# Kernel optimization log

Measured on AMD Instinct MI355X. Metric: run time of the kernel, lower is better.

Reference implementation:

```python
import jax, jax.numpy as jnp
import numpy as np

B, S, N_WIRES, EMBED_DIM, NUM_HEADS = 4, 2048, 8, 512, 8
D_K = EMBED_DIM // NUM_HEADS


def setup_inputs() -> dict:
    key = jax.random.key(0)
    k_x, k_th, k_q, k_k, k_v, k_c = jax.random.split(key, 6)
    x = jax.random.normal(k_x, (B, S, N_WIRES), dtype=jnp.float32)
    # trainable RX rotation angles, one per wire
    theta = jax.random.normal(k_th, (N_WIRES,), dtype=jnp.float32) * 0.1
    # nn.Linear(n_wires, embed_dim, bias=False) weights have shape (embed_dim, n_wires)
    sc_in = 1.0 / np.sqrt(N_WIRES)
    Wq = jax.random.normal(k_q, (EMBED_DIM, N_WIRES), dtype=jnp.float32) * sc_in
    Wk = jax.random.normal(k_k, (EMBED_DIM, N_WIRES), dtype=jnp.float32) * sc_in
    Wv = jax.random.normal(k_v, (EMBED_DIM, N_WIRES), dtype=jnp.float32) * sc_in
    Wc = jax.random.normal(k_c, (EMBED_DIM, EMBED_DIM), dtype=jnp.float32) * (1.0 / np.sqrt(EMBED_DIM))
    return {"x": x, "theta": theta, "Wq": Wq, "Wk": Wk, "Wv": Wv, "Wc": Wc}


def reference(x, theta, Wq, Wk, Wv, Wc):
    # Quantum encoding closed form: RX(x_i) then RX(theta_i) on |0> per wire gives <Z> = cos(x_i + theta_i).
    proj = jnp.cos(x + theta)  # (B, S, n_wires)
    b, s, _ = proj.shape
    q = jnp.einsum('bsn,en->bse', proj, Wq)
    k = jnp.einsum('bsn,en->bse', proj, Wk)
    v = jnp.einsum('bsn,en->bse', proj, Wv)
    # split heads: (B, H, S, d_k)
    q = q.reshape(b, s, NUM_HEADS, D_K).transpose(0, 2, 1, 3)
    k = k.reshape(b, s, NUM_HEADS, D_K).transpose(0, 2, 1, 3)
    v = v.reshape(b, s, NUM_HEADS, D_K).transpose(0, 2, 1, 3)
    scores = jnp.einsum('bhqd,bhkd->bhqk', q, k) / np.sqrt(D_K).astype(np.float32)
    attn = jax.nn.softmax(scores, axis=-1)  # dropout is identity at inference
    out = jnp.einsum('bhqk,bhkd->bhqd', attn, v)
    out = out.transpose(0, 2, 1, 3).reshape(b, s, EMBED_DIM)
    return jnp.einsum('bse,fe->bsf', out, Wc)
```

## Files before the change

### kernel.cpp

```cpp
#include <hip/hip_runtime.h>
#include <stdint.h>

#define N_B 4
#define S_LEN 2048
#define N_H 8
#define E_DIM 512

typedef __attribute__((ext_vector_type(8))) short bf16x8;
typedef __attribute__((ext_vector_type(4))) float f32x4;
typedef __attribute__((ext_vector_type(4))) unsigned int u32x4;
typedef __attribute__((ext_vector_type(2))) unsigned int u32x2;
typedef __attribute__((ext_vector_type(4))) unsigned short u16x4;
typedef __attribute__((ext_vector_type(8))) unsigned short u16x8;

#define MFMA16(a, b, c) __builtin_amdgcn_mfma_f32_16x16x32_bf16((a), (b), (c), 0, 0, 0)

__device__ __forceinline__ unsigned short f2bf(float f) {
    union { float f; unsigned int u; } v; v.f = f;
    unsigned int r = v.u + 0x7fffu + ((v.u >> 16) & 1u);
    return (unsigned short)(r >> 16);
}

__device__ __forceinline__ unsigned int pack2bf(float lo, float hi) {
    union { float f; unsigned int u; } a, b; a.f = lo; b.f = hi;
    return __builtin_amdgcn_perm(b.u + 0x8000u, a.u + 0x8000u, 0x07060302u);
}

__device__ __forceinline__ float fexp2(float x) {
#if __has_builtin(__builtin_amdgcn_exp2f)
    return __builtin_amdgcn_exp2f(x);
#else
    return exp2f(x);
#endif
}

#if __has_builtin(__builtin_amdgcn_permlane32_swap) && __has_builtin(__builtin_amdgcn_permlane16_swap)
#define HAVE_PERMLANE_SWAP 1
#endif

__device__ __forceinline__ void pl32(unsigned int& x, unsigned int& y) {
#ifdef HAVE_PERMLANE_SWAP
    auto r = __builtin_amdgcn_permlane32_swap(x, y, false, false);
    x = (unsigned int)r[0]; y = (unsigned int)r[1];
#else
    const int idx = (((int)threadIdx.x & 63) ^ 32) << 2;
    unsigned int xs = (unsigned int)__builtin_amdgcn_ds_bpermute(idx, (int)x);
    unsigned int ys = (unsigned int)__builtin_amdgcn_ds_bpermute(idx, (int)y);
    const bool lo = (threadIdx.x & 32) == 0;
    unsigned int nx = lo ? x : ys;
    unsigned int ny = lo ? xs : y;
    x = nx; y = ny;
#endif
}

__device__ __forceinline__ void pl16(unsigned int& x, unsigned int& y) {
#ifdef HAVE_PERMLANE_SWAP
    auto r = __builtin_amdgcn_permlane16_swap(x, y, false, false);
    x = (unsigned int)r[0]; y = (unsigned int)r[1];
#else
    unsigned int zs = (unsigned int)__builtin_amdgcn_ds_swizzle((int)y, 0x401F);
    unsigned int ws = (unsigned int)__builtin_amdgcn_ds_swizzle((int)x, 0x401F);
    const bool evenq = (threadIdx.x & 16) == 0;
    unsigned int nx = evenq ? x : zs;
    unsigned int ny = evenq ? ws : y;
    x = nx; y = ny;
#endif
}

#define Q_SCALE 0.18033688f

__global__ __launch_bounds__(256) void qkv_kernel(
    const float* __restrict__ x, const float* __restrict__ theta,
    const float* __restrict__ Wq, const float* __restrict__ Wk,
    const float* __restrict__ Wv,
    unsigned short* __restrict__ Q, unsigned short* __restrict__ K,
    unsigned short* __restrict__ Vt)
{
    __shared__ float proj[32][8];
    const int tid = threadIdx.x;
    const int mat = blockIdx.x % 3;
    const int chunk = blockIdx.x / 3;
    const int row0 = chunk * 32;
    const int b = row0 >> 11;
    const int s_in_b = row0 & (S_LEN - 1);

    proj[tid >> 3][tid & 7] = cosf(x[row0 * 8 + tid] + theta[tid & 7]);
    __syncthreads();

    if (mat < 2) {
        const float* W = (mat == 0) ? Wq : Wk;
        const float scale = (mat == 0) ? Q_SCALE : 1.0f;
        unsigned short* outp = (mat == 0) ? Q : K;
        const int eg = (tid & 127) * 4;
        const int sg = (tid >> 7) * 16;
        float w[4][8];
        #pragma unroll
        for (int e = 0; e < 4; ++e)
            #pragma unroll
            for (int n = 0; n < 8; ++n)
                w[e][n] = W[(eg + e) * 8 + n] * scale;
        const int h = eg >> 6, d0 = eg & 63;
        unsigned short* p0 = outp + ((size_t)(b * N_H + h) * S_LEN + s_in_b + sg) * 64 + d0;
        #pragma unroll 4
        for (int s = 0; s < 16; ++s) {
            f32x4 pa = *(const f32x4*)&proj[sg + s][0];
            f32x4 pc = *(const f32x4*)&proj[sg + s][4];
            u16x4 o;
            #pragma unroll
            for (int e = 0; e < 4; ++e) {
                float a = 0.f;
                #pragma unroll
                for (int n = 0; n < 4; ++n)
                    a += pa[n] * w[e][n] + pc[n] * w[e][n + 4];
                o[e] = f2bf(a);
            }
            *(u16x4*)&p0[s * 64] = o;
        }
    } else {
        f32x4 ps[8][2];
        const int sl0 = (tid & 3) * 8;
        #pragma unroll
        for (int k2 = 0; k2 < 8; ++k2) {
            ps[k2][0] = *(const f32x4*)&proj[sl0 + k2][0];
            ps[k2][1] = *(const f32x4*)&proj[sl0 + k2][4];
        }
        const int ecol = tid >> 2;
        for (int pass = 0; pass < 8; ++pass) {
            const int e = pass * 64 + ecol;
            const int h = e >> 6, dd = e & 63;
            float wr[8];
            #pragma unroll
            for (int n = 0; n < 8; ++n) wr[n] = Wv[e * 8 + n];
            u16x8 pk;
            #pragma unroll
            for (int k2 = 0; k2 < 8; ++k2) {
                float acc = 0.f;
                #pragma unroll
                for (int n = 0; n < 4; ++n)
                    acc += ps[k2][0][n] * wr[n] + ps[k2][1][n] * wr[n + 4];
                pk[k2] = f2bf(acc);
            }
            *(u16x8*)&Vt[((size_t)(b * N_H + h) * 64 + dd) * S_LEN + s_in_b + sl0] = pk;
        }
    }
}

__global__ __launch_bounds__(128) void flash_kernel(
    const unsigned short* __restrict__ Q, const unsigned short* __restrict__ K,
    const unsigned short* __restrict__ Vt, unsigned short* __restrict__ O)
{
    __shared__ short kt[2][64 * 72];
    __shared__ short vt[2][64 * 72];

    const int tid = threadIdx.x;
    const int lane = tid & 63, w = tid >> 6;
    const int quad = lane >> 4, lq = lane & 15;
    const int bid = (blockIdx.x & 7) * 64 + (blockIdx.x >> 3);
    const int qt = bid & 15, bh = bid >> 4;
    const int b = bh >> 3, h = bh & 7;

    const unsigned short* Qb = Q + (size_t)bh * S_LEN * 64;
    const unsigned short* Kb = K + (size_t)bh * S_LEN * 64;
    const unsigned short* Vb = Vt + (size_t)bh * 64 * S_LEN;

    bf16x8 qf[4][2];
    #pragma unroll
    for (int mt = 0; mt < 4; ++mt)
        #pragma unroll
        for (int ks = 0; ks < 2; ++ks)
            qf[mt][ks] = *(const bf16x8*)&Qb[(size_t)(qt * 128 + w * 64 + mt * 16 + lq) * 64 + ks * 32 + quad * 8];

    f32x4 oacc[4][4];
    #pragma unroll
    for (int mt = 0; mt < 4; ++mt)
        #pragma unroll
        for (int dt = 0; dt < 4; ++dt) oacc[mt][dt] = 0.f;
    float lsum[4] = {0.f, 0.f, 0.f, 0.f};

    u32x4 pkr[4], pvr[4];
    #pragma unroll
    for (int i = 0; i < 4; ++i) {
        const int u = tid + (i << 7);
        pkr[i] = *(const u32x4*)&Kb[(size_t)(u >> 3) * 64 + (u & 7) * 8];
        pvr[i] = *(const u32x4*)&Vb[(size_t)(u >> 3) * S_LEN + (u & 7) * 8];
    }
    #pragma unroll
    for (int i = 0; i < 4; ++i) {
        const int u = tid + (i << 7);
        *(u32x4*)&kt[0][(u >> 3) * 72 + (u & 7) * 8] = pkr[i];
        *(u32x4*)&vt[0][(u >> 3) * 72 + (u & 7) * 8] = pvr[i];
    }
    #pragma unroll
    for (int i = 0; i < 4; ++i) {
        const int u = tid + (i << 7);
        pkr[i] = *(const u32x4*)&Kb[(size_t)(64 + (u >> 3)) * 64 + (u & 7) * 8];
        pvr[i] = *(const u32x4*)&Vb[(size_t)(u >> 3) * S_LEN + 64 + (u & 7) * 8];
    }
    asm volatile("s_waitcnt lgkmcnt(0)" ::: "memory");
    __builtin_amdgcn_s_barrier();

    for (int kti = 0; kti < 32; ++kti) {
        const int cur = kti & 1, nxt = cur ^ 1;

        #pragma unroll
        for (int i = 0; i < 4; ++i) {
            const int u = tid + (i << 7);
            *(u32x4*)&kt[nxt][(u >> 3) * 72 + (u & 7) * 8] = pkr[i];
            *(u32x4*)&vt[nxt][(u >> 3) * 72 + (u & 7) * 8] = pvr[i];
        }
        const int kb2 = (kti < 30) ? (kti + 2) * 64 : 0;
        #pragma unroll
        for (int i = 0; i < 4; ++i) {
            const int u = tid + (i << 7);
            pkr[i] = *(const u32x4*)&Kb[(size_t)(kb2 + (u >> 3)) * 64 + (u & 7) * 8];
            pvr[i] = *(const u32x4*)&Vb[(size_t)(u >> 3) * S_LEN + kb2 + (u & 7) * 8];
        }

        const short* ktc = &kt[cur][0];
        const short* vtc = &vt[cur][0];

        #pragma unroll
        for (int ksub = 0; ksub < 2; ++ksub) {
            f32x4 sacc[4][2];
            #pragma unroll
            for (int mt = 0; mt < 4; ++mt)
                #pragma unroll
                for (int m2 = 0; m2 < 2; ++m2) sacc[mt][m2] = 0.f;
            #pragma unroll
            for (int m2 = 0; m2 < 2; ++m2) {
                #pragma unroll
                for (int ks = 0; ks < 2; ++ks) {
                    bf16x8 af = *(const bf16x8*)&ktc[((ksub * 2 + m2) * 16 + lq) * 72 + ks * 32 + quad * 8];
                    #pragma unroll
                    for (int mt = 0; mt < 4; ++mt)
                        sacc[mt][m2] = MFMA16(af, qf[mt][ks], sacc[mt][m2]);
                }
            }

            bf16x8 pa[4];
            #pragma unroll
            for (int mt = 0; mt < 4; ++mt) {
                unsigned int u_[2][2];
                #pragma unroll
                for (int m2 = 0; m2 < 2; ++m2) {
                    f32x4 p;
                    #pragma unroll
                    for (int e = 0; e < 4; ++e) p[e] = fexp2(sacc[mt][m2][e]);
                    lsum[mt] += (p[0] + p[1]) + (p[2] + p[3]);
                    u_[m2][0] = pack2bf(p[0], p[1]);
                    u_[m2][1] = pack2bf(p[2], p[3]);
                }
                union { unsigned int uu[4]; bf16x8 v; } A;
                #pragma unroll
                for (int wd = 0; wd < 2; ++wd) {
                    unsigned int a = u_[0][wd];
                    unsigned int c = u_[1][wd];
                    pl32(a, c);
                    pl16(a, c);
                    A.uu[wd] = a;
                    A.uu[2 + wd] = c;
                }
                pa[mt] = A.v;
            }

            #pragma unroll
            for (int dt = 0; dt < 4; ++dt) {
                bf16x8 bf = *(const bf16x8*)&vtc[(dt * 16 + lq) * 72 + ksub * 32 + quad * 8];
                #pragma unroll
                for (int mt = 0; mt < 4; ++mt)
                    oacc[mt][dt] = MFMA16(pa[mt], bf, oacc[mt][dt]);
            }
        }

        asm volatile("s_waitcnt lgkmcnt(0)" ::: "memory");
        __builtin_amdgcn_s_barrier();
    }

    #pragma unroll
    for (int mt = 0; mt < 4; ++mt) {
        float rs = lsum[mt];
        rs += __shfl_xor(rs, 16);
        rs += __shfl_xor(rs, 32);
        const float inv = 1.0f / rs;
        #pragma unroll
        for (int r = 0; r < 4; ++r) {
            const float ir = __shfl(inv, quad * 4 + r);
            const int row = qt * 128 + w * 64 + mt * 16 + quad * 4 + r;
            unsigned short* dst = &O[((size_t)b * S_LEN + row) * E_DIM + h * 64];
            #pragma unroll
            for (int dt = 0; dt < 4; ++dt)
                dst[dt * 16 + lq] = f2bf(oacc[mt][dt][r] * ir);
        }
    }
}

__global__ __launch_bounds__(256, 4) void outproj_kernel(
    const unsigned short* __restrict__ O, const float* __restrict__ Wc,
    float* __restrict__ Y)
{
    __shared__ short at[64 * 72];
    __shared__ short bt[64 * 72];
    const int tid = threadIdx.x;
    const int lane = tid & 63, w = tid >> 6;
    const int quad = lane >> 4, lq = lane & 15;
    const int m0 = (blockIdx.x >> 3) * 64;
    const int f0 = (blockIdx.x & 7) * 64;

    f32x4 acc[4];
    #pragma unroll
    for (int nt = 0; nt < 4; ++nt) acc[nt] = 0.f;

    u32x4 pa[2];
    f32x4 pw[4];
    #pragma unroll
    for (int i = 0; i < 2; ++i) {
        const int u = tid + (i << 8);
        pa[i] = *(const u32x4*)&O[(size_t)(m0 + (u >> 3)) * E_DIM + (u & 7) * 8];
    }
    #pragma unroll
    for (int i = 0; i < 4; ++i) {
        const int u = tid + (i << 8);
        pw[i] = *(const f32x4*)&Wc[(size_t)(f0 + (u >> 4)) * E_DIM + (u & 15) * 4];
    }

    for (int e0 = 0; e0 < E_DIM; e0 += 64) {
        __syncthreads();
        #pragma unroll
        for (int i = 0; i < 2; ++i) {
            const int u = tid + (i << 8);
            *(u32x4*)&at[(u >> 3) * 72 + (u & 7) * 8] = pa[i];
        }
        #pragma unroll
        for (int i = 0; i < 4; ++i) {
            const int u = tid + (i << 8);
            u16x4 pk = { f2bf(pw[i][0]), f2bf(pw[i][1]), f2bf(pw[i][2]), f2bf(pw[i][3]) };
            *(u16x4*)&bt[(u >> 4) * 72 + (u & 15) * 4] = pk;
        }
        __syncthreads();

        const int e1 = (e0 + 64 < E_DIM) ? e0 + 64 : 0;
        #pragma unroll
        for (int i = 0; i < 2; ++i) {
            const int u = tid + (i << 8);
            pa[i] = *(const u32x4*)&O[(size_t)(m0 + (u >> 3)) * E_DIM + e1 + (u & 7) * 8];
        }
        #pragma unroll
        for (int i = 0; i < 4; ++i) {
            const int u = tid + (i << 8);
            pw[i] = *(const f32x4*)&Wc[(size_t)(f0 + (u >> 4)) * E_DIM + e1 + (u & 15) * 4];
        }

        bf16x8 afk[2];
        #pragma unroll
        for (int ks = 0; ks < 2; ++ks)
            afk[ks] = *(const bf16x8*)&at[(w * 16 + lq) * 72 + ks * 32 + quad * 8];
        #pragma unroll
        for (int nt = 0; nt < 4; ++nt) {
            #pragma unroll
            for (int ks = 0; ks < 2; ++ks) {
                bf16x8 bf = *(const bf16x8*)&bt[(nt * 16 + lq) * 72 + ks * 32 + quad * 8];
                acc[nt] = MFMA16(afk[ks], bf, acc[nt]);
            }
        }
    }

    #pragma unroll
    for (int nt = 0; nt < 4; ++nt)
        #pragma unroll
        for (int r = 0; r < 4; ++r)
            Y[(size_t)(m0 + w * 16 + quad * 4 + r) * E_DIM + f0 + nt * 16 + lq] = acc[nt][r];
}

extern "C" void kernel_launch(void* const* d_in, const int* in_sizes, int n_in,
                              void* d_out, int out_size, void* d_ws, size_t ws_size,
                              hipStream_t stream) {
    const float* x     = (const float*)d_in[0];
    const float* theta = (const float*)d_in[1];
    const float* Wq    = (const float*)d_in[2];
    const float* Wk    = (const float*)d_in[3];
    const float* Wv    = (const float*)d_in[4];
    const float* Wc    = (const float*)d_in[5];
    float* Y = (float*)d_out;

    char* ws = (char*)d_ws;
    unsigned short* Q  = (unsigned short*)(ws);
    unsigned short* K  = (unsigned short*)(ws + ((size_t)8 << 20));
    unsigned short* Vt = (unsigned short*)(ws + ((size_t)16 << 20));
    unsigned short* O  = (unsigned short*)(ws + ((size_t)24 << 20));

    qkv_kernel<<<(N_B * S_LEN / 32) * 3, 256, 0, stream>>>(x, theta, Wq, Wk, Wv, Q, K, Vt);
    flash_kernel<<<N_B * N_H * (S_LEN / 128), 128, 0, stream>>>(Q, K, Vt, O);
    outproj_kernel<<<(N_B * S_LEN / 64) * (E_DIM / 64), 256, 0, stream>>>(O, Wc, Y);
}
```

Baseline: 153.5 us.

## Split key range across two wave groups in flash kernel and merge via LDS

The flash attention block grows from 2 to 4 waves. Each pair of waves handles the same 128 query rows but only half of the key/value sequence, using its own double-buffered LDS tiles. At the end, the second group writes its partial output accumulators and row sums to LDS, and the first group adds them before normalizing and storing. The aim is to double the number of resident waves and halve the serial key loop per block. The cost is more LDS per block and an extra reduction step with a block-wide barrier.

```diff
diff --git a/kernel.cpp b/kernel.cpp
--- a/kernel.cpp
+++ b/kernel.cpp
@@ -145,15 +145,18 @@
     }
 }
 
-__global__ __launch_bounds__(128) void flash_kernel(
+__global__ __launch_bounds__(256, 2) void flash_kernel(
     const unsigned short* __restrict__ Q, const unsigned short* __restrict__ K,
     const unsigned short* __restrict__ Vt, unsigned short* __restrict__ O)
 {
-    __shared__ short kt[2][64 * 72];
-    __shared__ short vt[2][64 * 72];
+    __shared__ short kt[2][2][64 * 72];
+    __shared__ short vt[2][2][64 * 72];
 
     const int tid = threadIdx.x;
     const int lane = tid & 63, w = tid >> 6;
+    const int g = w >> 1;
+    const int wq = w & 1;
+    const int tgl = tid & 127;
     const int quad = lane >> 4, lq = lane & 15;
     const int bid = (blockIdx.x & 7) * 64 + (blockIdx.x >> 3);
     const int qt = bid & 15, bh = bid >> 4;
@@ -162,13 +165,14 @@
     const unsigned short* Qb = Q + (size_t)bh * S_LEN * 64;
     const unsigned short* Kb = K + (size_t)bh * S_LEN * 64;
     const unsigned short* Vb = Vt + (size_t)bh * 64 * S_LEN;
+    const int kbase = g * 1024;
 
     bf16x8 qf[4][2];
     #pragma unroll
     for (int mt = 0; mt < 4; ++mt)
         #pragma unroll
         for (int ks = 0; ks < 2; ++ks)
-            qf[mt][ks] = *(const bf16x8*)&Qb[(size_t)(qt * 128 + w * 64 + mt * 16 + lq) * 64 + ks * 32 + quad * 8];
+            qf[mt][ks] = *(const bf16x8*)&Qb[(size_t)(qt * 128 + wq * 64 + mt * 16 + lq) * 64 + ks * 32 + quad * 8];
 
     f32x4 oacc[4][4];
     #pragma unroll
@@ -180,44 +184,44 @@
     u32x4 pkr[4], pvr[4];
     #pragma unroll
     for (int i = 0; i < 4; ++i) {
-        const int u = tid + (i << 7);
-        pkr[i] = *(const u32x4*)&Kb[(size_t)(u >> 3) * 64 + (u & 7) * 8];
-        pvr[i] = *(const u32x4*)&Vb[(size_t)(u >> 3) * S_LEN + (u & 7) * 8];
+        const int u = tgl + (i << 7);
+        pkr[i] = *(const u32x4*)&Kb[(size_t)(kbase + (u >> 3)) * 64 + (u & 7) * 8];
+        pvr[i] = *(const u32x4*)&Vb[(size_t)(u >> 3) * S_LEN + kbase + (u & 7) * 8];
     }
     #pragma unroll
     for (int i = 0; i < 4; ++i) {
-        const int u = tid + (i << 7);
-        *(u32x4*)&kt[0][(u >> 3) * 72 + (u & 7) * 8] = pkr[i];
-        *(u32x4*)&vt[0][(u >> 3) * 72 + (u & 7) * 8] = pvr[i];
+        const int u = tgl + (i << 7);
+        *(u32x4*)&kt[g][0][(u >> 3) * 72 + (u & 7) * 8] = pkr[i];
+        *(u32x4*)&vt[g][0][(u >> 3) * 72 + (u & 7) * 8] = pvr[i];
     }
     #pragma unroll
     for (int i = 0; i < 4; ++i) {
-        const int u = tid + (i << 7);
-        pkr[i] = *(const u32x4*)&Kb[(size_t)(64 + (u >> 3)) * 64 + (u & 7) * 8];
-        pvr[i] = *(const u32x4*)&Vb[(size_t)(u >> 3) * S_LEN + 64 + (u & 7) * 8];
+        const int u = tgl + (i << 7);
+        pkr[i] = *(const u32x4*)&Kb[(size_t)(kbase + 64 + (u >> 3)) * 64 + (u & 7) * 8];
+        pvr[i] = *(const u32x4*)&Vb[(size_t)(u >> 3) * S_LEN + kbase + 64 + (u & 7) * 8];
     }
     asm volatile("s_waitcnt lgkmcnt(0)" ::: "memory");
     __builtin_amdgcn_s_barrier();
 
-    for (int kti = 0; kti < 32; ++kti) {
+    for (int kti = 0; kti < 16; ++kti) {
         const int cur = kti & 1, nxt = cur ^ 1;
 
         #pragma unroll
         for (int i = 0; i < 4; ++i) {
-            const int u = tid + (i << 7);
-            *(u32x4*)&kt[nxt][(u >> 3) * 72 + (u & 7) * 8] = pkr[i];
-            *(u32x4*)&vt[nxt][(u >> 3) * 72 + (u & 7) * 8] = pvr[i];
-        }
-        const int kb2 = (kti < 30) ? (kti + 2) * 64 : 0;
+            const int u = tgl + (i << 7);
+            *(u32x4*)&kt[g][nxt][(u >> 3) * 72 + (u & 7) * 8] = pkr[i];
+            *(u32x4*)&vt[g][nxt][(u >> 3) * 72 + (u & 7) * 8] = pvr[i];
+        }
+        const int kb2 = kbase + ((kti < 14) ? (kti + 2) * 64 : 0);
         #pragma unroll
         for (int i = 0; i < 4; ++i) {
-            const int u = tid + (i << 7);
+            const int u = tgl + (i << 7);
             pkr[i] = *(const u32x4*)&Kb[(size_t)(kb2 + (u >> 3)) * 64 + (u & 7) * 8];
             pvr[i] = *(const u32x4*)&Vb[(size_t)(u >> 3) * S_LEN + kb2 + (u & 7) * 8];
         }
 
-        const short* ktc = &kt[cur][0];
-        const short* vtc = &vt[cur][0];
+        const short* ktc = &kt[g][cur][0];
+        const short* vtc = &vt[g][cur][0];
 
         #pragma unroll
         for (int ksub = 0; ksub < 2; ++ksub) {
@@ -276,20 +280,45 @@
         __builtin_amdgcn_s_barrier();
     }
 
-    #pragma unroll
-    for (int mt = 0; mt < 4; ++mt) {
-        float rs = lsum[mt];
-        rs += __shfl_xor(rs, 16);
-        rs += __shfl_xor(rs, 32);
-        const float inv = 1.0f / rs;
-        #pragma unroll
-        for (int r = 0; r < 4; ++r) {
-            const float ir = __shfl(inv, quad * 4 + r);
-            const int row = qt * 128 + w * 64 + mt * 16 + quad * 4 + r;
-            unsigned short* dst = &O[((size_t)b * S_LEN + row) * E_DIM + h * 64];
+    float* exO = (float*)&kt[0][0][0];
+    float* exL = (float*)&vt[0][0][0];
+    const int fb = (wq * 64 + lane) * 68;
+    if (g == 1) {
+        #pragma unroll
+        for (int mt = 0; mt < 4; ++mt)
             #pragma unroll
             for (int dt = 0; dt < 4; ++dt)
-                dst[dt * 16 + lq] = f2bf(oacc[mt][dt][r] * ir);
+                *(f32x4*)&exO[fb + (mt * 4 + dt) * 4] = oacc[mt][dt];
+        #pragma unroll
+        for (int mt = 0; mt < 4; ++mt)
+            exL[(wq * 64 + lane) * 4 + mt] = lsum[mt];
+    }
+    __syncthreads();
+    if (g == 0) {
+        #pragma unroll
+        for (int mt = 0; mt < 4; ++mt)
+            #pragma unroll
+            for (int dt = 0; dt < 4; ++dt)
+                oacc[mt][dt] += *(const f32x4*)&exO[fb + (mt * 4 + dt) * 4];
+        #pragma unroll
+        for (int mt = 0; mt < 4; ++mt)
+            lsum[mt] += exL[(wq * 64 + lane) * 4 + mt];
+
+        #pragma unroll
+        for (int mt = 0; mt < 4; ++mt) {
+            float rs = lsum[mt];
+            rs += __shfl_xor(rs, 16);
+            rs += __shfl_xor(rs, 32);
+            const float inv = 1.0f / rs;
+            #pragma unroll
+            for (int r = 0; r < 4; ++r) {
+                const float ir = __shfl(inv, quad * 4 + r);
+                const int row = qt * 128 + wq * 64 + mt * 16 + quad * 4 + r;
+                unsigned short* dst = &O[((size_t)b * S_LEN + row) * E_DIM + h * 64];
+                #pragma unroll
+                for (int dt = 0; dt < 4; ++dt)
+                    dst[dt * 16 + lq] = f2bf(oacc[mt][dt][r] * ir);
+            }
         }
     }
 }
@@ -389,6 +418,6 @@
     unsigned short* O  = (unsigned short*)(ws + ((size_t)24 << 20));
 
     qkv_kernel<<<(N_B * S_LEN / 32) * 3, 256, 0, stream>>>(x, theta, Wq, Wk, Wv, Q, K, Vt);
-    flash_kernel<<<N_B * N_H * (S_LEN / 128), 128, 0, stream>>>(Q, K, Vt, O);
+    flash_kernel<<<N_B * N_H * (S_LEN / 128), 256, 0, stream>>>(Q, K, Vt, O);
     outproj_kernel<<<(N_B * S_LEN / 64) * (E_DIM / 64), 256, 0, stream>>>(O, Wc, Y);
 }
```

After: 140.0 us. 1.1x faster.
